# Performance work log

Measured on AMD Instinct MI355X. Metric: run time of the kernel, lower is better.

The kernel has to match this reference:

```python
import jax, jax.numpy as jnp
import numpy as np

B, S, D, H, F, L, V = 8, 512, 768, 12, 3072, 12, 30522
DK = D // H
SCALE = 1.0 / float(np.sqrt(DK))


def _ln(x, g, b, eps):
    mu = jnp.mean(x, -1, keepdims=True)
    var = jnp.mean((x - mu) ** 2, -1, keepdims=True)
    return (x - mu) / jnp.sqrt(var + eps) * g + b


def setup_inputs() -> dict:
    key = jax.random.key(0)
    ks = jax.random.split(key, 16)
    s = 0.02
    d = {
        'input_ids': jax.random.randint(ks[0], (B, S), 0, V),
        'token_type_ids': jax.random.randint(ks[1], (B, S), 0, 2),
        'attention_mask': jnp.ones((B, S), jnp.float32),
        'word_emb': jax.random.normal(ks[2], (V, D), jnp.float32) * s,
        'pos_emb': jax.random.normal(ks[3], (512, D), jnp.float32) * s,
        'type_emb': jax.random.normal(ks[4], (2, D), jnp.float32) * s,
        'emb_ln_g': jnp.ones((D,), jnp.float32),
        'emb_ln_b': jnp.zeros((D,), jnp.float32),
        # per-layer stacked params (torch Linear convention: W is [out,in])
        'Wq': jax.random.normal(ks[5], (L, D, D), jnp.float32) * s,
        'bq': jnp.zeros((L, D), jnp.float32),
        'Wk': jax.random.normal(ks[6], (L, D, D), jnp.float32) * s,
        'bk': jnp.zeros((L, D), jnp.float32),
        'Wv': jax.random.normal(ks[7], (L, D, D), jnp.float32) * s,
        'bv': jnp.zeros((L, D), jnp.float32),
        'Wo': jax.random.normal(ks[8], (L, D, D), jnp.float32) * s,
        'bo': jnp.zeros((L, D), jnp.float32),
        'attn_ln_g': jnp.ones((L, D), jnp.float32),
        'attn_ln_b': jnp.zeros((L, D), jnp.float32),
        'W1': jax.random.normal(ks[9], (L, F, D), jnp.float32) * s,
        'b1': jnp.zeros((L, F), jnp.float32),
        'W2': jax.random.normal(ks[10], (L, D, F), jnp.float32) * s,
        'b2': jnp.zeros((L, D), jnp.float32),
        'ffn_ln_g': jnp.ones((L, D), jnp.float32),
        'ffn_ln_b': jnp.zeros((L, D), jnp.float32),
    }
    return d


def reference(input_ids, token_type_ids, attention_mask, word_emb, pos_emb,
              type_emb, emb_ln_g, emb_ln_b, Wq, bq, Wk, bk, Wv, bv, Wo, bo,
              attn_ln_g, attn_ln_b, W1, b1, W2, b2, ffn_ln_g, ffn_ln_b):
    # Embeddings (dropout = identity in eval)
    x = word_emb[input_ids] + type_emb[token_type_ids] + pos_emb[:S][None]
    x = _ln(x, emb_ln_g, emb_ln_b, 1e-12)

    mask0 = attention_mask[:, None, None, :] == 0  # (B,1,1,S)

    def step(x, p):
        wq, bq_, wk, bk_, wv, bv_, wo, bo_, ag, ab, w1, b1_, w2, b2_, fg, fb = p
        q = (jnp.einsum('bsd,ed->bse', x, wq) + bq_).reshape(B, S, H, DK).transpose(0, 2, 1, 3)
        k = (jnp.einsum('bsd,ed->bse', x, wk) + bk_).reshape(B, S, H, DK).transpose(0, 2, 1, 3)
        v = (jnp.einsum('bsd,ed->bse', x, wv) + bv_).reshape(B, S, H, DK).transpose(0, 2, 1, 3)
        attn = jnp.einsum('bhqd,bhkd->bhqk', q, k) * SCALE  # (B,H,S,S)
        attn = jnp.where(mask0, -1e9, attn)
        p_attn = jax.nn.softmax(attn, axis=-1)
        ctx = jnp.einsum('bhqk,bhkd->bhqd', p_attn, v).transpose(0, 2, 1, 3).reshape(B, S, D)
        a = _ln(jnp.einsum('bsd,ed->bse', ctx, wo) + bo_ + x, ag, ab, 1e-5)
        # FFN: NO activation, and final LN has NO residual (faithful to source)
        h = jnp.einsum('bsd,fd->bsf', a, w1) + b1_
        y = jnp.einsum('bsf,df->bsd', h, w2) + b2_
        return _ln(y, fg, fb, 1e-5), None

    x, _ = jax.lax.scan(step, x, (Wq, bq, Wk, bk, Wv, bv, Wo, bo,
                                  attn_ln_g, attn_ln_b, W1, b1, W2, b2,
                                  ffn_ln_g, ffn_ln_b))
    return x
```

## Files before the change

### kernel.cpp

```cpp
#include <hip/hip_runtime.h>
#include <hip/hip_bf16.h>
#include <cstdint>
#include <cstddef>

typedef __bf16 bf16;
typedef __bf16 bf16x8 __attribute__((ext_vector_type(8)));
typedef __bf16 bf16x4 __attribute__((ext_vector_type(4)));
typedef float  floatx4 __attribute__((ext_vector_type(4)));

__device__ __forceinline__ void gload_lds16(const bf16* g, bf16* l) {
    __builtin_amdgcn_global_load_lds((const __attribute__((address_space(1))) void*)g,
                                     (__attribute__((address_space(3))) void*)l, 16, 0, 0);
}

__device__ __forceinline__ floatx4 mfma16(bf16x8 a, bf16x8 b, floatx4 c) {
    return __builtin_amdgcn_mfma_f32_16x16x32_bf16(a, b, c, 0, 0, 0);
}

template<int MODE, int TN>
__global__ __launch_bounds__(256)
void gemm_bt(const bf16* __restrict__ A, const bf16* __restrict__ Bw,
             const float* __restrict__ bias0, const float* __restrict__ bias1,
             const float* __restrict__ bias2,
             float* __restrict__ Cf, bf16* __restrict__ Cb0,
             bf16* __restrict__ Cb1, bf16* __restrict__ Cb2,
             int M, int N, int K)
{
    constexpr int NJ = TN / 32;
    __shared__ __attribute__((aligned(16))) bf16 As[128 * 32];
    __shared__ __attribute__((aligned(16))) bf16 Bs[TN * 32];

    const int tid  = threadIdx.x;
    const int lane = tid & 63;
    const int wv   = tid >> 6;
    const int quad = lane >> 4;
    const int l16  = lane & 15;
    const int m0   = blockIdx.y * 128;
    const int n0   = blockIdx.x * TN;
    const int wm   = wv & 1;
    const int wn   = wv >> 1;

    floatx4 acc[4][NJ] = {};

    const int srow = lane >> 2;
    const int scol = (lane & 3) * 8;
    const bf16* gA0 = A  + (size_t)(m0 + wv * 16 + srow) * K + scol;
    const bf16* gA1 = gA0 + (size_t)64 * K;
    const bf16* gB0 = Bw + (size_t)(n0 + wv * 16 + srow) * K + scol;
    const bf16* gB1 = gB0 + (size_t)64 * K;
    bf16* lA0 = &As[wv * 512];
    bf16* lA1 = &As[2048 + wv * 512];
    bf16* lB0 = &Bs[wv * 512];
    bf16* lB1 = &Bs[2048 + wv * 512];

    for (int k0 = 0; k0 < K; k0 += 32) {
        gload_lds16(gA0 + k0, lA0);
        gload_lds16(gA1 + k0, lA1);
        gload_lds16(gB0 + k0, lB0);
        if (TN == 128) gload_lds16(gB1 + k0, lB1);
        __syncthreads();

        bf16x8 af[4], bfr[NJ];
        #pragma unroll
        for (int i = 0; i < 4; ++i)
            af[i] = *(const bf16x8*)&As[(wm * 64 + i * 16 + l16) * 32 + quad * 8];
        #pragma unroll
        for (int j = 0; j < NJ; ++j)
            bfr[j] = *(const bf16x8*)&Bs[(wn * NJ * 16 + j * 16 + l16) * 32 + quad * 8];

        #pragma unroll
        for (int i = 0; i < 4; ++i)
            #pragma unroll
            for (int j = 0; j < NJ; ++j)
                acc[i][j] = mfma16(af[i], bfr[j], acc[i][j]);
        __syncthreads();
    }

    #pragma unroll
    for (int i = 0; i < 4; ++i) {
        const int rbase = m0 + wm * 64 + i * 16 + quad * 4;
        #pragma unroll
        for (int j = 0; j < NJ; ++j) {
            const int col = n0 + wn * NJ * 16 + j * 16 + l16;
            if (MODE == 0) {
                const float bv = bias0[col];
                #pragma unroll
                for (int r = 0; r < 4; ++r)
                    Cf[(size_t)(rbase + r) * N + col] = acc[i][j][r] + bv;
            } else if (MODE == 1) {
                const float bv = bias0[col];
                #pragma unroll
                for (int r = 0; r < 4; ++r)
                    Cb0[(size_t)(rbase + r) * N + col] = (bf16)(acc[i][j][r] + bv);
            } else {
                const int sel = col / 768;
                const int cc  = col - sel * 768;
                if (sel < 2) {
                    bf16* dst = (sel == 0) ? Cb0 : Cb1;
                    const float bv = ((sel == 0) ? bias0 : bias1)[cc];
                    #pragma unroll
                    for (int r = 0; r < 4; ++r)
                        dst[(size_t)(rbase + r) * 768 + cc] = (bf16)(acc[i][j][r] + bv);
                } else {
                    const float bv = bias2[cc];
                    const int bb = rbase >> 9, s = rbase & 511;
                    const int h = cc >> 6, d = cc & 63;
                    bf16x4 o;
                    #pragma unroll
                    for (int r = 0; r < 4; ++r) o[r] = (bf16)(acc[i][j][r] + bv);
                    *(bf16x4*)(Cb2 + (((size_t)(bb * 12 + h) * 64 + d) * 512 + s)) = o;
                }
            }
        }
    }
}

__global__ __launch_bounds__(256)
void cvt_all(const float* __restrict__ Wq, const float* __restrict__ Wk,
             const float* __restrict__ Wv, const float* __restrict__ Wo,
             const float* __restrict__ W1, const float* __restrict__ W2,
             bf16* __restrict__ out)
{
    const int l = blockIdx.y;
    const size_t i = ((size_t)blockIdx.x * 256 + threadIdx.x) * 4;
    const size_t wdd = 589824, wdf = 2359296;
    const float* src;
    size_t off;
    if      (i <  589824) { src = Wq + l * wdd; off = i; }
    else if (i < 1179648) { src = Wk + l * wdd; off = i - 589824; }
    else if (i < 1769472) { src = Wv + l * wdd; off = i - 1179648; }
    else if (i < 2359296) { src = Wo + l * wdd; off = i - 1769472; }
    else if (i < 4718592) { src = W1 + l * wdf; off = i - 2359296; }
    else                  { src = W2 + l * wdf; off = i - 4718592; }
    const float4 v = *(const float4*)(src + off);
    bf16x4 o;
    o[0] = (bf16)v.x; o[1] = (bf16)v.y; o[2] = (bf16)v.z; o[3] = (bf16)v.w;
    *(bf16x4*)(out + (size_t)l * 7077888 + i) = o;
}

__global__ __launch_bounds__(256)
void attn3(const bf16* __restrict__ Q, const bf16* __restrict__ Kb,
           const bf16* __restrict__ VT, const float* __restrict__ mask,
           bf16* __restrict__ CTX)
{
    __shared__ __attribute__((aligned(16))) bf16 Ks[64 * 64];
    __shared__ __attribute__((aligned(16))) bf16 Vs[64 * 64];
    __shared__ __attribute__((aligned(16))) bf16 Ps[4 * 16 * 72];
    __shared__ float mb[512];

    const int tid  = threadIdx.x;
    const int lane = tid & 63;
    const int w    = tid >> 6;
    const int quad = lane >> 4;
    const int l16  = lane & 15;
    const int qt = blockIdx.x, h = blockIdx.y, b = blockIdx.z;

    mb[tid]       = (mask[b * 512 + tid] == 0.f)       ? -1e9f : -16.0f;
    mb[tid + 256] = (mask[b * 512 + tid + 256] == 0.f) ? -1e9f : -16.0f;

    bf16x8 qf0, qf1;
    {
        const bf16* qp = Q + (size_t)(b * 512 + qt * 64 + w * 16 + l16) * 768 + h * 64;
        qf0 = *(const bf16x8*)(qp + quad * 8);
        qf1 = *(const bf16x8*)(qp + 32 + quad * 8);
    }

    float lsum[4] = {0.f, 0.f, 0.f, 0.f};
    floatx4 accO[4] = {};
    bf16* pw = &Ps[w * 1152];

    const int srow8 = lane >> 3;
    const int scol8 = (lane & 7) * 8;

    for (int kt = 0; kt < 8; ++kt) {
        #pragma unroll
        for (int i = 0; i < 2; ++i) {
            const int r0 = w * 16 + i * 8;
            gload_lds16(Kb + (size_t)(b * 512 + kt * 64 + r0 + srow8) * 768 + h * 64 + scol8,
                        &Ks[r0 * 64]);
            gload_lds16(VT + ((size_t)(b * 12 + h) * 64 + r0 + srow8) * 512 + kt * 64 + scol8,
                        &Vs[r0 * 64]);
        }
        __syncthreads();

        #pragma unroll
        for (int ct = 0; ct < 4; ++ct) {
            const bf16x8 kf0 = *(const bf16x8*)&Ks[(ct * 16 + l16) * 64 + quad * 8];
            const bf16x8 kf1 = *(const bf16x8*)&Ks[(ct * 16 + l16) * 64 + 32 + quad * 8];
            floatx4 a = {0.f, 0.f, 0.f, 0.f};
            a = mfma16(qf0, kf0, a);
            a = mfma16(qf1, kf1, a);
            const float mbv = mb[kt * 64 + ct * 16 + l16];
            #pragma unroll
            for (int r = 0; r < 4; ++r) {
                const float p = __expf(fmaf(a[r], 0.125f, mbv));
                lsum[r] += p;
                pw[(quad * 4 + r) * 72 + ct * 16 + l16] = (bf16)p;
            }
        }

        #pragma unroll
        for (int kc = 0; kc < 2; ++kc) {
            const bf16x8 af = *(const bf16x8*)&pw[l16 * 72 + kc * 32 + quad * 8];
            #pragma unroll
            for (int ct2 = 0; ct2 < 4; ++ct2) {
                const bf16x8 bv = *(const bf16x8*)&Vs[(ct2 * 16 + l16) * 64 + kc * 32 + quad * 8];
                accO[ct2] = mfma16(af, bv, accO[ct2]);
            }
        }
        __syncthreads();
    }

    float inv[4];
    #pragma unroll
    for (int r = 0; r < 4; ++r) {
        float s = lsum[r];
        #pragma unroll
        for (int o = 1; o < 16; o <<= 1) s += __shfl_xor(s, o);
        inv[r] = 1.0f / s;
    }
    #pragma unroll
    for (int ct2 = 0; ct2 < 4; ++ct2)
        #pragma unroll
        for (int r = 0; r < 4; ++r) {
            const int row = qt * 64 + w * 16 + quad * 4 + r;
            CTX[(size_t)(b * 512 + row) * 768 + h * 64 + ct2 * 16 + l16] =
                (bf16)(accO[ct2][r] * inv[r]);
        }
}

__global__ __launch_bounds__(256)
void embed_ln_k(const int* __restrict__ ids, const int* __restrict__ tts,
                const float* __restrict__ we, const float* __restrict__ pe,
                const float* __restrict__ te, const float* __restrict__ g,
                const float* __restrict__ b, float* __restrict__ X,
                bf16* __restrict__ XB)
{
    __shared__ float red[4];
    const int row = blockIdx.x;
    const int s   = row & 511;
    const int tid = threadIdx.x;
    const int id  = ids[row];
    const int tt  = tts[row];
    const float* pwp = we + (size_t)id * 768;
    const float* pt = te + (size_t)tt * 768;
    const float* pp = pe + (size_t)s * 768;
    const size_t base = (size_t)row * 768;

    float v[3];
    #pragma unroll
    for (int j = 0; j < 3; ++j) {
        const int c = tid + j * 256;
        v[j] = pwp[c] + pt[c] + pp[c];
    }
    float sm = v[0] + v[1] + v[2];
    for (int o = 32; o; o >>= 1) sm += __shfl_down(sm, o);
    if ((tid & 63) == 0) red[tid >> 6] = sm;
    __syncthreads();
    const float mu = (red[0] + red[1] + red[2] + red[3]) * (1.0f / 768.0f);
    float q = 0.f;
    #pragma unroll
    for (int j = 0; j < 3; ++j) { const float d = v[j] - mu; q += d * d; }
    __syncthreads();
    for (int o = 32; o; o >>= 1) q += __shfl_down(q, o);
    if ((tid & 63) == 0) red[tid >> 6] = q;
    __syncthreads();
    const float var  = (red[0] + red[1] + red[2] + red[3]) * (1.0f / 768.0f);
    const float rstd = rsqrtf(var + 1e-12f);
    #pragma unroll
    for (int j = 0; j < 3; ++j) {
        const int c = tid + j * 256;
        const float o = (v[j] - mu) * rstd * g[c] + b[c];
        X[base + c]  = o;
        XB[base + c] = (bf16)o;
    }
}

__global__ __launch_bounds__(256)
void ln_k(const float* T, const float* res, const float* g, const float* bta,
          float* Xo, bf16* XBo)
{
    __shared__ float red[4];
    const int row = blockIdx.x;
    const int tid = threadIdx.x;
    const size_t base = (size_t)row * 768;

    float v[3];
    #pragma unroll
    for (int j = 0; j < 3; ++j) {
        const int c = tid + j * 256;
        float x = T[base + c];
        if (res) x += res[base + c];
        v[j] = x;
    }
    float sm = v[0] + v[1] + v[2];
    for (int o = 32; o; o >>= 1) sm += __shfl_down(sm, o);
    if ((tid & 63) == 0) red[tid >> 6] = sm;
    __syncthreads();
    const float mu = (red[0] + red[1] + red[2] + red[3]) * (1.0f / 768.0f);
    float q = 0.f;
    #pragma unroll
    for (int j = 0; j < 3; ++j) { const float d = v[j] - mu; q += d * d; }
    __syncthreads();
    for (int o = 32; o; o >>= 1) q += __shfl_down(q, o);
    if ((tid & 63) == 0) red[tid >> 6] = q;
    __syncthreads();
    const float var  = (red[0] + red[1] + red[2] + red[3]) * (1.0f / 768.0f);
    const float rstd = rsqrtf(var + 1e-5f);
    #pragma unroll
    for (int j = 0; j < 3; ++j) {
        const int c = tid + j * 256;
        const float o = (v[j] - mu) * rstd * g[c] + bta[c];
        Xo[base + c]  = o;
        XBo[base + c] = (bf16)o;
    }
}

extern "C" void kernel_launch(void* const* d_in, const int* in_sizes, int n_in,
                              void* d_out, int out_size, void* d_ws, size_t ws_size,
                              hipStream_t stream)
{
    const int*   ids  = (const int*)d_in[0];
    const int*   tts  = (const int*)d_in[1];
    const float* mask = (const float*)d_in[2];
    const float* wemb = (const float*)d_in[3];
    const float* pemb = (const float*)d_in[4];
    const float* temb = (const float*)d_in[5];
    const float* eg   = (const float*)d_in[6];
    const float* eb   = (const float*)d_in[7];
    const float* Wq   = (const float*)d_in[8];
    const float* bq   = (const float*)d_in[9];
    const float* Wk   = (const float*)d_in[10];
    const float* bk   = (const float*)d_in[11];
    const float* Wv   = (const float*)d_in[12];
    const float* bv   = (const float*)d_in[13];
    const float* Wo   = (const float*)d_in[14];
    const float* bo   = (const float*)d_in[15];
    const float* ag   = (const float*)d_in[16];
    const float* ab   = (const float*)d_in[17];
    const float* W1   = (const float*)d_in[18];
    const float* b1   = (const float*)d_in[19];
    const float* W2   = (const float*)d_in[20];
    const float* b2   = (const float*)d_in[21];
    const float* fg   = (const float*)d_in[22];
    const float* fb   = (const float*)d_in[23];

    char* p = (char*)d_ws;
    float* X   = (float*)p; p += 12582912;
    bf16* XB   = (bf16*)p;  p += 6291456;
    bf16* Qb   = (bf16*)p;  p += 6291456;
    bf16* Kbuf = (bf16*)p;  p += 6291456;
    bf16* CTXb = (bf16*)p;  p += 6291456;
    float* T1  = (float*)p; p += 12582912;
    bf16* HB   = (bf16*)p;  p += 25165824;
    bf16* WB   = (bf16*)p;  p += 169869312;
    bf16* VT   = HB;

    cvt_all<<<dim3(6912, 12), 256, 0, stream>>>(Wq, Wk, Wv, Wo, W1, W2, WB);
    embed_ln_k<<<4096, 256, 0, stream>>>(ids, tts, wemb, pemb, temb, eg, eb, X, XB);

    for (int l = 0; l < 12; ++l) {
        bf16* wb = WB + (size_t)l * 7077888;
        gemm_bt<2, 128><<<dim3(18, 32), 256, 0, stream>>>(
            XB, wb, bq + l * 768, bk + l * 768, bv + l * 768,
            nullptr, Qb, Kbuf, VT, 4096, 2304, 768);
        attn3<<<dim3(8, 12, 8), 256, 0, stream>>>(Qb, Kbuf, VT, mask, CTXb);
        gemm_bt<0, 64><<<dim3(12, 32), 256, 0, stream>>>(
            CTXb, wb + 1769472, bo + l * 768, nullptr, nullptr,
            T1, nullptr, nullptr, nullptr, 4096, 768, 768);
        ln_k<<<4096, 256, 0, stream>>>(T1, X, ag + l * 768, ab + l * 768, X, XB);
        gemm_bt<1, 128><<<dim3(24, 32), 256, 0, stream>>>(
            XB, wb + 2359296, b1 + (size_t)l * 3072, nullptr, nullptr,
            nullptr, HB, nullptr, nullptr, 4096, 3072, 768);
        gemm_bt<0, 64><<<dim3(12, 32), 256, 0, stream>>>(
            HB, wb + 4718592, b2 + l * 768, nullptr, nullptr,
            T1, nullptr, nullptr, nullptr, 4096, 768, 3072);
        float* outX = (l == 11) ? (float*)d_out : X;
        ln_k<<<4096, 256, 0, stream>>>(T1, nullptr, fg + l * 768, fb + l * 768, outX, XB);
    }
}
```

Measured before the change: 2.646 ms.

## Double-buffer K/V tiles with swizzled LDS in attention and widen weight conversion

The attention kernel now keeps two LDS buffers for K and V tiles. It prefetches the next tile right after the barrier, which drops one barrier per iteration and overlaps global loads with MFMA work. Column indices are XOR-swizzled by row to reduce LDS bank conflicts on fragment reads. The weight conversion kernel now processes 8 elements per thread with half the grid. The cost is doubled LDS for K/V, which may lower occupancy.

```diff
diff --git a/kernel.cpp b/kernel.cpp
--- a/kernel.cpp
+++ b/kernel.cpp
@@ -122,7 +122,7 @@
              bf16* __restrict__ out)
 {
     const int l = blockIdx.y;
-    const size_t i = ((size_t)blockIdx.x * 256 + threadIdx.x) * 4;
+    const size_t i = ((size_t)blockIdx.x * 256 + threadIdx.x) * 8;
     const size_t wdd = 589824, wdf = 2359296;
     const float* src;
     size_t off;
@@ -132,10 +132,12 @@
     else if (i < 2359296) { src = Wo + l * wdd; off = i - 1769472; }
     else if (i < 4718592) { src = W1 + l * wdf; off = i - 2359296; }
     else                  { src = W2 + l * wdf; off = i - 4718592; }
-    const float4 v = *(const float4*)(src + off);
-    bf16x4 o;
-    o[0] = (bf16)v.x; o[1] = (bf16)v.y; o[2] = (bf16)v.z; o[3] = (bf16)v.w;
-    *(bf16x4*)(out + (size_t)l * 7077888 + i) = o;
+    const float4 v0 = *(const float4*)(src + off);
+    const float4 v1 = *(const float4*)(src + off + 4);
+    bf16x8 o;
+    o[0] = (bf16)v0.x; o[1] = (bf16)v0.y; o[2] = (bf16)v0.z; o[3] = (bf16)v0.w;
+    o[4] = (bf16)v1.x; o[5] = (bf16)v1.y; o[6] = (bf16)v1.z; o[7] = (bf16)v1.w;
+    *(bf16x8*)(out + (size_t)l * 7077888 + i) = o;
 }
 
 __global__ __launch_bounds__(256)
@@ -143,8 +145,8 @@
            const bf16* __restrict__ VT, const float* __restrict__ mask,
            bf16* __restrict__ CTX)
 {
-    __shared__ __attribute__((aligned(16))) bf16 Ks[64 * 64];
-    __shared__ __attribute__((aligned(16))) bf16 Vs[64 * 64];
+    __shared__ __attribute__((aligned(16))) bf16 Ks[2][64 * 64];
+    __shared__ __attribute__((aligned(16))) bf16 Vs[2][64 * 64];
     __shared__ __attribute__((aligned(16))) bf16 Ps[4 * 16 * 72];
     __shared__ float mb[512];
 
@@ -170,23 +172,32 @@
     bf16* pw = &Ps[w * 1152];
 
     const int srow8 = lane >> 3;
-    const int scol8 = (lane & 7) * 8;
+    const int scol8 = ((lane & 7) * 8) ^ (srow8 << 3);
+    const int r0b   = w * 16;
+
+    auto stageKV = [&](int kt, int bi) {
+        #pragma unroll
+        for (int i = 0; i < 2; ++i) {
+            const int r0 = r0b + i * 8;
+            gload_lds16(Kb + (size_t)(b * 512 + kt * 64 + r0 + srow8) * 768 + h * 64 + scol8,
+                        &Ks[bi][r0 * 64]);
+            gload_lds16(VT + ((size_t)(b * 12 + h) * 64 + r0 + srow8) * 512 + kt * 64 + scol8,
+                        &Vs[bi][r0 * 64]);
+        }
+    };
+
+    stageKV(0, 0);
+    int cur = 0;
+    const int swm = (l16 & 7) << 3;
 
     for (int kt = 0; kt < 8; ++kt) {
-        #pragma unroll
-        for (int i = 0; i < 2; ++i) {
-            const int r0 = w * 16 + i * 8;
-            gload_lds16(Kb + (size_t)(b * 512 + kt * 64 + r0 + srow8) * 768 + h * 64 + scol8,
-                        &Ks[r0 * 64]);
-            gload_lds16(VT + ((size_t)(b * 12 + h) * 64 + r0 + srow8) * 512 + kt * 64 + scol8,
-                        &Vs[r0 * 64]);
-        }
         __syncthreads();
+        if (kt < 7) stageKV(kt + 1, cur ^ 1);
 
         #pragma unroll
         for (int ct = 0; ct < 4; ++ct) {
-            const bf16x8 kf0 = *(const bf16x8*)&Ks[(ct * 16 + l16) * 64 + quad * 8];
-            const bf16x8 kf1 = *(const bf16x8*)&Ks[(ct * 16 + l16) * 64 + 32 + quad * 8];
+            const bf16x8 kf0 = *(const bf16x8*)&Ks[cur][(ct * 16 + l16) * 64 + ((quad * 8) ^ swm)];
+            const bf16x8 kf1 = *(const bf16x8*)&Ks[cur][(ct * 16 + l16) * 64 + ((quad * 8 + 32) ^ swm)];
             floatx4 a = {0.f, 0.f, 0.f, 0.f};
             a = mfma16(qf0, kf0, a);
             a = mfma16(qf1, kf1, a);
@@ -204,11 +215,11 @@
             const bf16x8 af = *(const bf16x8*)&pw[l16 * 72 + kc * 32 + quad * 8];
             #pragma unroll
             for (int ct2 = 0; ct2 < 4; ++ct2) {
-                const bf16x8 bv = *(const bf16x8*)&Vs[(ct2 * 16 + l16) * 64 + kc * 32 + quad * 8];
+                const bf16x8 bv = *(const bf16x8*)&Vs[cur][(ct2 * 16 + l16) * 64 + ((kc * 32 + quad * 8) ^ swm)];
                 accO[ct2] = mfma16(af, bv, accO[ct2]);
             }
         }
-        __syncthreads();
+        cur ^= 1;
     }
 
     float inv[4];
@@ -356,7 +367,7 @@
     bf16* WB   = (bf16*)p;  p += 169869312;
     bf16* VT   = HB;
 
-    cvt_all<<<dim3(6912, 12), 256, 0, stream>>>(Wq, Wk, Wv, Wo, W1, W2, WB);
+    cvt_all<<<dim3(3456, 12), 256, 0, stream>>>(Wq, Wk, Wv, Wo, W1, W2, WB);
     embed_ln_k<<<4096, 256, 0, stream>>>(ids, tts, wemb, pemb, temb, eg, eb, X, XB);
 
     for (int l = 0; l < 12; ++l) {
```

Result: no change. 2.621 ms (-0.9%).
